# Optimization experiments

Measured on AMD Instinct MI355X. Metric: run time of the kernel, lower is better.

The kernel has to match this reference:

```python
import jax, jax.numpy as jnp
import numpy as np

B, S, D = 2, 2048, 2048
H, G = 32, 8           # num_heads, num_groups
HD = D // H            # head_dim = 64
GS = H // G            # group_size = 4


def setup_inputs() -> dict:
    key = jax.random.key(0)
    ks = jax.random.split(key, 11)
    s = 0.02
    return {
        "x": jax.random.normal(ks[0], (B, S, D), dtype=jnp.float32),
        "kv": jax.random.normal(ks[1], (B, S, D), dtype=jnp.float32),
        "Wq": jax.random.normal(ks[2], (D, D), dtype=jnp.float32) * s,
        "bq": jnp.zeros((D,), dtype=jnp.float32),
        "Wk": jax.random.normal(ks[3], (D, G * HD), dtype=jnp.float32) * s,
        "bk": jnp.zeros((G * HD,), dtype=jnp.float32),
        "Wv": jax.random.normal(ks[4], (D, G * HD), dtype=jnp.float32) * s,
        "bv": jnp.zeros((G * HD,), dtype=jnp.float32),
        "Wo": jax.random.normal(ks[5], (D, D), dtype=jnp.float32) * s,
        "bo": jnp.zeros((D,), dtype=jnp.float32),
        "expanding_context": 0,
    }


def reference(x, kv, Wq, bq, Wk, bk, Wv, bv, Wo, bo, expanding_context):
    # expanding_context is ignored when use_kv_cache=False (matches torch module)
    b, s, d = x.shape
    q = (x @ Wq + bq).reshape(b, s, H, HD).transpose(0, 2, 1, 3)      # [B,H,S,HD]
    k = (kv @ Wk + bk).reshape(b, s, G, HD).transpose(0, 2, 1, 3)     # [B,G,S,HD]
    v = (kv @ Wv + bv).reshape(b, s, G, HD).transpose(0, 2, 1, 3)     # [B,G,S,HD]
    # repeat_interleave KV heads to match query heads
    k = jnp.repeat(k, GS, axis=1)                                      # [B,H,S,HD]
    v = jnp.repeat(v, GS, axis=1)
    scale = 1.0 / jnp.sqrt(jnp.array(HD, dtype=x.dtype))
    scores = jnp.einsum("bhqd,bhkd->bhqk", q, k) * scale              # [B,H,S,S]
    causal = jnp.tril(jnp.ones((s, s), dtype=bool))                    # True where allowed
    scores = jnp.where(causal[None, None], scores, jnp.finfo(x.dtype).min)
    attn = jax.nn.softmax(scores, axis=-1)
    out = jnp.einsum("bhqk,bhkd->bhqd", attn, v)                      # [B,H,S,HD]
    out = out.transpose(0, 2, 1, 3).reshape(b, s, D)                  # [B,S,D]
    return out @ Wo + bo
```

## Files before the change

kernel.cpp:

```cpp
#include <hip/hip_runtime.h>
#include <hip/hip_bf16.h>
#include <stdint.h>

namespace {
constexpr int CB = 2, CS = 2048, CD = 2048, CH = 32, CG = 8, CHD = 64, CGS = 4;

typedef __bf16 bf16x8 __attribute__((ext_vector_type(8)));
typedef float f32x4 __attribute__((ext_vector_type(4)));
typedef float f32x16 __attribute__((ext_vector_type(16)));
typedef uint32_t u32x4 __attribute__((ext_vector_type(4)));

__device__ inline uint16_t f2bf(float f) {
  uint32_t u = __float_as_uint(f);
  u += 0x7fffu + ((u >> 16) & 1u);
  return (uint16_t)(u >> 16);
}

__device__ inline void gload_lds16(const void* g, void* l) {
  __builtin_amdgcn_global_load_lds(
      (const __attribute__((address_space(1))) void*)g,
      (__attribute__((address_space(3))) void*)l, 16, 0, 0);
}

__device__ inline uint32_t cvtpk_bf16(float lo, float hi) {
  uint32_t r;
  asm("v_cvt_pk_bf16_f32 %0, %1, %2" : "=v"(r) : "v"(lo), "v"(hi));
  return r;
}
__device__ inline void pl32swap(uint32_t& a, uint32_t& b) {
  asm("v_permlane32_swap_b32 %0, %1" : "+v"(a), "+v"(b));
}
}

__global__ __launch_bounds__(256) void cast_both_kernel(
    const float* __restrict__ x, const float* __restrict__ kv,
    uint16_t* __restrict__ xb, uint16_t* __restrict__ kvb, int nel) {
  int i = (blockIdx.x * 256 + threadIdx.x) * 4;
  const float* in;
  uint16_t* out;
  if (i < nel) { in = x + i; out = xb + i; }
  else         { in = kv + (i - nel); out = kvb + (i - nel); }
  const float4 v = *(const float4*)in;
  ushort4 o;
  o.x = f2bf(v.x); o.y = f2bf(v.y); o.z = f2bf(v.z); o.w = f2bf(v.w);
  *(ushort4*)out = o;
}

__global__ __launch_bounds__(256) void transpose_all_kernel(
    const float* __restrict__ Wq, const float* __restrict__ Wk,
    const float* __restrict__ Wv, const float* __restrict__ Wo,
    uint16_t* __restrict__ out) {
  __shared__ uint16_t tile[32][33];
  const int gn0 = blockIdx.x * 32;
  const int k0 = blockIdx.y * 32;
  const float* in;
  int Nr, start;
  if (gn0 < 2048)      { in = Wq; Nr = 2048; start = 0; }
  else if (gn0 < 2560) { in = Wk; Nr = 512;  start = 2048; }
  else if (gn0 < 3072) { in = Wv; Nr = 512;  start = 2560; }
  else                 { in = Wo; Nr = 2048; start = 3072; }
  const int n0 = gn0 - start;
  const int tx = threadIdx.x & 31, tg = threadIdx.x >> 5;
#pragma unroll
  for (int rr = 0; rr < 4; ++rr) {
    int k = tg * 4 + rr;
    tile[k][tx] = f2bf(in[(size_t)(k0 + k) * Nr + n0 + tx]);
  }
  __syncthreads();
#pragma unroll
  for (int rr = 0; rr < 4; ++rr) {
    int n = tg * 4 + rr;
    out[(size_t)(gn0 + n) * CD + k0 + tx] = tile[tx][n];
  }
}

__global__ __launch_bounds__(512, 2) void gemm_qkv_kernel(
    const uint16_t* __restrict__ xb, const uint16_t* __restrict__ kvb,
    const uint16_t* __restrict__ WT,
    const float* __restrict__ bq, const float* __restrict__ bk,
    const float* __restrict__ bv,
    uint16_t* __restrict__ Qb, uint16_t* __restrict__ Kb,
    uint16_t* __restrict__ VTb) {
  constexpr int BM = 256, BN = 256, BK = 32, K = 2048, NT = K / BK;
  constexpr int ASZ = BM * BK;
  constexpr int BSZ = BN * BK;
  constexpr int BUFSZ = ASZ + BSZ;
  __shared__ uint16_t smem[3 * BUFSZ];
  const int tid = threadIdx.x;
  const int w = tid >> 6, l = tid & 63;
  const int wr = w >> 2, wc = w & 3;
  const int l15 = l & 15, lq = l >> 4;

  const int gx = gridDim.x;
  int bid = blockIdx.y * gx + blockIdx.x;
  const int nwg = gx * gridDim.y;
  bid = (bid & 7) * (nwg >> 3) + (bid >> 3);
  const int m0 = (bid / gx) * BM, n0 = (bid % gx) * BN;
  const uint16_t* A = (n0 < 2048) ? xb : kvb;

  auto stage = [&](int buf, int kt) {
    uint16_t* base = smem + buf * BUFSZ;
    const int k0 = kt * BK;
#pragma unroll
    for (int i = 0; i < 2; ++i) {
      int g = i * 512 + tid;
      int row = g >> 2, slot = g & 3;
      int kq = slot ^ (row & 3);
      gload_lds16(A + (size_t)(m0 + row) * K + k0 + kq * 8, base + g * 8);
    }
#pragma unroll
    for (int i = 0; i < 2; ++i) {
      int g = i * 512 + tid;
      int row = g >> 2, slot = g & 3;
      int kq = slot ^ (row & 3);
      gload_lds16(WT + (size_t)(n0 + row) * K + k0 + kq * 8,
                  base + ASZ + g * 8);
    }
  };

  int aOff[8], bOff[4];
#pragma unroll
  for (int m = 0; m < 8; ++m) {
    int row = wr * 128 + m * 16 + l15;
    aOff[m] = (row * BK + (lq ^ (row & 3)) * 8) * 2;
  }
#pragma unroll
  for (int n = 0; n < 4; ++n) {
    int row = wc * 64 + n * 16 + l15;
    bOff[n] = ASZ * 2 + (row * BK + (lq ^ (row & 3)) * 8) * 2;
  }

  f32x4 acc[8][4] = {};

  stage(0, 0);
  stage(1, 1);

  int bt = 0, bs = 2;
  for (int t = 0; t < NT; ++t) {
    if (t < NT - 1) asm volatile("s_waitcnt vmcnt(4)" ::: "memory");
    else            asm volatile("s_waitcnt vmcnt(0)" ::: "memory");
    __builtin_amdgcn_s_barrier();
    asm volatile("" ::: "memory");

    const char* buf = (const char*)(smem + bt * BUFSZ);
    bf16x8 af[8], bfr[4];
#pragma unroll
    for (int m = 0; m < 8; ++m) af[m] = *(const bf16x8*)(buf + aOff[m]);
#pragma unroll
    for (int n = 0; n < 4; ++n) bfr[n] = *(const bf16x8*)(buf + bOff[n]);

    if (t + 2 < NT) stage(bs, t + 2);

    __builtin_amdgcn_s_setprio(1);
#pragma unroll
    for (int m = 0; m < 8; ++m)
#pragma unroll
      for (int n = 0; n < 4; ++n)
        acc[m][n] = __builtin_amdgcn_mfma_f32_16x16x32_bf16(
            af[m], bfr[n], acc[m][n], 0, 0, 0);
    __builtin_amdgcn_s_setprio(0);

    bt = bt == 2 ? 0 : bt + 1;
    bs = bs == 2 ? 0 : bs + 1;
  }

#pragma unroll
  for (int m = 0; m < 8; ++m)
#pragma unroll
    for (int n = 0; n < 4; ++n)
#pragma unroll
      for (int r = 0; r < 4; ++r) {
        int gm = m0 + wr * 128 + m * 16 + lq * 4 + r;
        int gn = n0 + wc * 64 + n * 16 + l15;
        int b = gm >> 11, s = gm & (CS - 1);
        if (n0 < 2048) {
          float v = (acc[m][n][r] + bq[gn]) * (0.125f * 1.44269504088896340736f);
          int h = gn >> 6, hd = gn & 63;
          Qb[(((size_t)(b * CH + h)) * CS + s) * CHD + hd] = f2bf(v);
        } else if (n0 < 2560) {
          int gn2 = gn - 2048;
          float v = acc[m][n][r] + bk[gn2];
          int gh = gn2 >> 6, hd = gn2 & 63;
          Kb[(((size_t)(b * CG + gh)) * CS + s) * CHD + hd] = f2bf(v);
        } else {
          int gn2 = gn - 2560;
          float v = acc[m][n][r] + bv[gn2];
          int gh = gn2 >> 6, hd = gn2 & 63;
          VTb[(((size_t)(b * CG + gh)) * CHD + hd) * CS + s] = f2bf(v);
        }
      }
}

__global__ __launch_bounds__(512, 2) void gemm_out_kernel(
    const uint16_t* __restrict__ A, const uint16_t* __restrict__ Bt,
    const float* __restrict__ bias, float* __restrict__ Cout,
    int M, int N, int Kdim) {
  constexpr int BM = 256, BN = 128, BK = 32, K = 2048, NT = K / BK;
  constexpr int ASZ = BM * BK;
  constexpr int BSZ = BN * BK;
  constexpr int BUFSZ = ASZ + BSZ;
  __shared__ uint16_t smem[3 * BUFSZ];
  const int tid = threadIdx.x;
  const int w = tid >> 6, l = tid & 63;
  const int wr = w >> 2, wc = w & 3;
  const int l15 = l & 15, lq = l >> 4;

  const int gx = gridDim.x;
  int bid = blockIdx.y * gx + blockIdx.x;
  const int nwg = gx * gridDim.y;
  bid = (bid & 7) * (nwg >> 3) + (bid >> 3);
  const int m0 = (bid / gx) * BM, n0 = (bid % gx) * BN;

  auto stage = [&](int buf, int kt) {
    uint16_t* base = smem + buf * BUFSZ;
    const int k0 = kt * BK;
#pragma unroll
    for (int i = 0; i < 2; ++i) {
      int g = i * 512 + tid;
      int row = g >> 2, slot = g & 3;
      int kq = slot ^ (row & 3);
      gload_lds16(A + (size_t)(m0 + row) * K + k0 + kq * 8, base + g * 8);
    }
    {
      int g = tid;
      int row = g >> 2, slot = g & 3;
      int kq = slot ^ (row & 3);
      gload_lds16(Bt + (size_t)(n0 + row) * K + k0 + kq * 8,
                  base + ASZ + g * 8);
    }
  };

  int aOff[8], bOff[2];
#pragma unroll
  for (int m = 0; m < 8; ++m) {
    int row = wr * 128 + m * 16 + l15;
    aOff[m] = (row * BK + (lq ^ (row & 3)) * 8) * 2;
  }
#pragma unroll
  for (int n = 0; n < 2; ++n) {
    int row = wc * 32 + n * 16 + l15;
    bOff[n] = ASZ * 2 + (row * BK + (lq ^ (row & 3)) * 8) * 2;
  }

  f32x4 acc[8][2] = {};

  stage(0, 0);
  stage(1, 1);

  int bt = 0, bs = 2;
  for (int t = 0; t < NT; ++t) {
    if (t < NT - 1) asm volatile("s_waitcnt vmcnt(3)" ::: "memory");
    else            asm volatile("s_waitcnt vmcnt(0)" ::: "memory");
    __builtin_amdgcn_s_barrier();
    asm volatile("" ::: "memory");

    const char* buf = (const char*)(smem + bt * BUFSZ);
    bf16x8 af[8], bfr[2];
#pragma unroll
    for (int m = 0; m < 8; ++m) af[m] = *(const bf16x8*)(buf + aOff[m]);
#pragma unroll
    for (int n = 0; n < 2; ++n) bfr[n] = *(const bf16x8*)(buf + bOff[n]);

    if (t + 2 < NT) stage(bs, t + 2);

    __builtin_amdgcn_s_setprio(1);
#pragma unroll
    for (int m = 0; m < 8; ++m)
#pragma unroll
      for (int n = 0; n < 2; ++n)
        acc[m][n] = __builtin_amdgcn_mfma_f32_16x16x32_bf16(
            af[m], bfr[n], acc[m][n], 0, 0, 0);
    __builtin_amdgcn_s_setprio(0);

    bt = bt == 2 ? 0 : bt + 1;
    bs = bs == 2 ? 0 : bs + 1;
  }

#pragma unroll
  for (int m = 0; m < 8; ++m)
#pragma unroll
    for (int n = 0; n < 2; ++n)
#pragma unroll
      for (int r = 0; r < 4; ++r) {
        int gm = m0 + wr * 128 + m * 16 + lq * 4 + r;
        int gn = n0 + wc * 32 + n * 16 + l15;
        Cout[(size_t)gm * N + gn] = acc[m][n][r] + bias[gn];
      }
}

__global__ __launch_bounds__(256) void flash_attn_kernel(
    const uint16_t* __restrict__ Q, const uint16_t* __restrict__ K,
    const uint16_t* __restrict__ VT, uint16_t* __restrict__ Aout) {
  constexpr int NQB = CS / 128;
  __shared__ __align__(16) uint16_t Ksm[2][64 * 64];
  __shared__ __align__(16) uint16_t Vsm[2][64 * 64];
  const int tid = threadIdx.x, w = tid >> 6, l = tid & 63;
  const int l31 = l & 31, hi = l >> 5;
  const int x = blockIdx.x;
  const int h = blockIdx.y, b = blockIdx.z, g = h >> 2;

  const uint16_t* Qbase = Q + ((size_t)(b * CH + h)) * CS * CHD;
  const uint16_t* Kbase = K + ((size_t)(b * CG + g)) * CS * CHD;
  const uint16_t* Vbase = VT + ((size_t)(b * CG + g)) * CHD * CS;

  const int srow = tid >> 3, sslot = tid & 7;
  const int skq = sslot ^ (srow & 7);
  const uint16_t* kSrc0 = Kbase + (size_t)srow * CHD + skq * 8;
  const uint16_t* kSrc1 = kSrc0 + 32 * CHD;
  const uint16_t* vSrc0 = Vbase + (size_t)srow * CS + skq * 8;
  const uint16_t* vSrc1 = vSrc0 + 32 * CS;
  uint16_t* kDst0 = &Ksm[0][0] + tid * 8;
  uint16_t* vDst0 = &Vsm[0][0] + tid * 8;

  int qkOff[2][4];
#pragma unroll
  for (int c = 0; c < 2; ++c)
#pragma unroll
    for (int kc = 0; kc < 4; ++kc) {
      int row = c * 32 + l31;
      qkOff[c][kc] = ((row * 64 + kc * 16 + hi * 8) * 2) ^ ((row & 7) << 4);
    }

  auto stage = [&](int buf, int kt) {
    const size_t ko = (size_t)kt * 64 * CHD;
    const int vo = kt * 64;
    uint16_t* kd = kDst0 + buf * 64 * 64;
    uint16_t* vd = vDst0 + buf * 64 * 64;
    gload_lds16(kSrc0 + ko, kd);
    gload_lds16(kSrc1 + ko, kd + 2048);
    gload_lds16(vSrc0 + vo, vd);
    gload_lds16(vSrc1 + vo, vd + 2048);
  };

#pragma unroll 1
  for (int job = 0; job < 2; ++job) {
    const int qb = job == 0 ? (NQB - 1 - x) : x;
    const int qrow = qb * 128 + w * 32 + l31;
    const int wtop = qb * 128 + w * 32 + 31;

    bf16x8 qf[4];
#pragma unroll
    for (int kc = 0; kc < 4; ++kc)
      qf[kc] = *(const bf16x8*)(Qbase + (size_t)qrow * CHD + kc * 16 + hi * 8);

    f32x16 o0 = {}, o1 = {};
    float mrun = -3e38f, lrun = 0.f;
    const int nt = 2 * qb + 2;

    stage(0, 0);
    asm volatile("s_waitcnt vmcnt(0)" ::: "memory");
    __syncthreads();

    for (int kt = 0; kt < nt; ++kt) {
      const int cur = kt & 1;
      if (kt + 1 < nt) stage(cur ^ 1, kt + 1);

      if (kt * 64 <= wtop) {
        const char* ksmb = (const char*)Ksm[cur];
        const char* vsmb = (const char*)Vsm[cur];

        f32x16 p0 = {}, p1 = {};
        __builtin_amdgcn_s_setprio(1);
#pragma unroll
        for (int kc = 0; kc < 4; ++kc) {
          bf16x8 ka0 = *(const bf16x8*)(ksmb + qkOff[0][kc]);
          bf16x8 ka1 = *(const bf16x8*)(ksmb + qkOff[1][kc]);
          p0 = __builtin_amdgcn_mfma_f32_32x32x16_bf16(ka0, qf[kc], p0, 0, 0, 0);
          p1 = __builtin_amdgcn_mfma_f32_32x32x16_bf16(ka1, qf[kc], p1, 0, 0, 0);
        }
        __builtin_amdgcn_s_setprio(0);

        const bool need_mask = (kt * 64 + 63 > qb * 128 + w * 32);
        float pmax = -3e38f;
        if (need_mask) {
#pragma unroll
          for (int r = 0; r < 16; ++r) {
            int keyb = kt * 64 + (r & 3) + 8 * (r >> 2) + 4 * hi;
            if (keyb > qrow) p0[r] = -3e38f;
            if (keyb + 32 > qrow) p1[r] = -3e38f;
          }
        }
#pragma unroll
        for (int r = 0; r < 16; ++r) {
          pmax = fmaxf(pmax, p0[r]);
          pmax = fmaxf(pmax, p1[r]);
        }
        pmax = fmaxf(pmax, __shfl_xor(pmax, 32));

        if (!__all(pmax <= mrun + 8.f)) {
          float mnew = fmaxf(mrun, pmax);
          float alpha = __builtin_amdgcn_exp2f(mrun - mnew);
#pragma unroll
          for (int r = 0; r < 16; ++r) { o0[r] *= alpha; o1[r] *= alpha; }
          lrun *= alpha;
          mrun = mnew;
        }
        float s = 0.f;
#pragma unroll
        for (int r = 0; r < 16; ++r) {
          float e0 = __builtin_amdgcn_exp2f(p0[r] - mrun);
          float e1 = __builtin_amdgcn_exp2f(p1[r] - mrun);
          p0[r] = e0; p1[r] = e1;
          s += e0 + e1;
        }
        s += __shfl_xor(s, 32);
        lrun += s;

        u32x4 paw[4];
#pragma unroll
        for (int k = 0; k < 4; ++k) {
          const int base = (k & 1) * 8;
          const f32x16& pc = (k >> 1) ? p1 : p0;
          uint32_t c01 = cvtpk_bf16(pc[base + 0], pc[base + 1]);
          uint32_t c23 = cvtpk_bf16(pc[base + 2], pc[base + 3]);
          uint32_t c45 = cvtpk_bf16(pc[base + 4], pc[base + 5]);
          uint32_t c67 = cvtpk_bf16(pc[base + 6], pc[base + 7]);
          pl32swap(c01, c45);
          pl32swap(c23, c67);
          paw[k] = (u32x4){c01, c23, c45, c67};
        }

        __builtin_amdgcn_s_setprio(1);
#pragma unroll
        for (int ks = 0; ks < 4; ++ks) {
          bf16x8 vb0 = *(const bf16x8*)(vsmb + qkOff[0][ks]);
          bf16x8 vb1 = *(const bf16x8*)(vsmb + qkOff[1][ks]);
          bf16x8 pb = __builtin_bit_cast(bf16x8, paw[ks]);
          o0 = __builtin_amdgcn_mfma_f32_32x32x16_bf16(vb0, pb, o0, 0, 0, 0);
          o1 = __builtin_amdgcn_mfma_f32_32x32x16_bf16(vb1, pb, o1, 0, 0, 0);
        }
        __builtin_amdgcn_s_setprio(0);
      }

      asm volatile("s_waitcnt vmcnt(0)" ::: "memory");
      __syncthreads();
    }

    float invl = 1.f / lrun;
    uint16_t* orow = Aout + ((size_t)b * CS + qrow) * CD + (size_t)h * CHD;
#pragma unroll
    for (int k = 0; k < 8; ++k) {
      int reg = 2 * k;
      int hd = (reg & 3) + 8 * (reg >> 2) + 4 * hi;
      *(uint32_t*)(orow + hd) = cvtpk_bf16(o0[reg] * invl, o0[reg + 1] * invl);
      *(uint32_t*)(orow + hd + 32) = cvtpk_bf16(o1[reg] * invl, o1[reg + 1] * invl);
    }
  }
}

extern "C" void kernel_launch(void* const* d_in, const int* in_sizes, int n_in,
                              void* d_out, int out_size, void* d_ws, size_t ws_size,
                              hipStream_t stream) {
  const float* x = (const float*)d_in[0];
  const float* kv = (const float*)d_in[1];
  const float* Wq = (const float*)d_in[2];
  const float* bq = (const float*)d_in[3];
  const float* Wk = (const float*)d_in[4];
  const float* bk = (const float*)d_in[5];
  const float* Wv = (const float*)d_in[6];
  const float* bv = (const float*)d_in[7];
  const float* Wo = (const float*)d_in[8];
  const float* bo = (const float*)d_in[9];
  float* out = (float*)d_out;

  char* ws = (char*)d_ws;
  uint16_t* xb = (uint16_t*)ws;   ws += (size_t)CB * CS * CD * 2;
  uint16_t* kvb = (uint16_t*)ws;  ws += (size_t)CB * CS * CD * 2;
  uint16_t* WqT = (uint16_t*)ws;  ws += (size_t)CD * CD * 2;
  uint16_t* WkT = (uint16_t*)ws;  ws += (size_t)(CG * CHD) * CD * 2;
  uint16_t* WvT = (uint16_t*)ws;  ws += (size_t)(CG * CHD) * CD * 2;
  uint16_t* WoT = (uint16_t*)ws;  ws += (size_t)CD * CD * 2;
  uint16_t* Qb = (uint16_t*)ws;   ws += (size_t)CB * CH * CS * CHD * 2;
  uint16_t* Kb = (uint16_t*)ws;   ws += (size_t)CB * CG * CS * CHD * 2;
  uint16_t* VTb = (uint16_t*)ws;  ws += (size_t)CB * CG * CHD * CS * 2;
  uint16_t* attnb = (uint16_t*)ws;
  (void)WkT; (void)WvT;

  const int NTOK = CB * CS;
  const int nel = CB * CS * CD;

  cast_both_kernel<<<2 * nel / 4 / 256, 256, 0, stream>>>(x, kv, xb, kvb, nel);
  transpose_all_kernel<<<dim3(5120 / 32, CD / 32), 256, 0, stream>>>(
      Wq, Wk, Wv, Wo, WqT);

  gemm_qkv_kernel<<<dim3(3072 / 256, NTOK / 256), 512, 0, stream>>>(
      xb, kvb, WqT, bq, bk, bv, Qb, Kb, VTb);

  flash_attn_kernel<<<dim3(CS / 256, CH, CB), 256, 0, stream>>>(Qb, Kb, VTb, attnb);

  gemm_out_kernel<<<dim3(CD / 128, NTOK / 256), 512, 0, stream>>>(
      attnb, WoT, bo, out, NTOK, CD, CD);
}
```

Before: 217.6 us.

## Split GEMM k-step into two half-phases with interleaved staging and new LDS swizzle

Both projection GEMM kernels now split each k-iteration into two halves. A-tile prefetch is issued after the first half's fragment loads and B-tile prefetch after the second half's, with an extra barrier in between. This spreads global-to-LDS traffic across the MFMA work and lowers register pressure from fragments. The LDS XOR swizzle also changes from row&3 to (row>>1)&3 to cut bank conflicts on the 16-byte reads. The extra barrier per iteration adds sync cost. The wait counts at loop top are unchanged even though issue order now differs, so prefetch accounting may be tighter.

```diff
diff --git a/kernel.cpp b/kernel.cpp
--- a/kernel.cpp
+++ b/kernel.cpp
@@ -98,21 +98,25 @@
   const int m0 = (bid / gx) * BM, n0 = (bid % gx) * BN;
   const uint16_t* A = (n0 < 2048) ? xb : kvb;
 
-  auto stage = [&](int buf, int kt) {
+  auto stageA = [&](int buf, int kt) {
     uint16_t* base = smem + buf * BUFSZ;
     const int k0 = kt * BK;
 #pragma unroll
     for (int i = 0; i < 2; ++i) {
       int g = i * 512 + tid;
       int row = g >> 2, slot = g & 3;
-      int kq = slot ^ (row & 3);
+      int kq = slot ^ ((row >> 1) & 3);
       gload_lds16(A + (size_t)(m0 + row) * K + k0 + kq * 8, base + g * 8);
     }
+  };
+  auto stageB = [&](int buf, int kt) {
+    uint16_t* base = smem + buf * BUFSZ;
+    const int k0 = kt * BK;
 #pragma unroll
     for (int i = 0; i < 2; ++i) {
       int g = i * 512 + tid;
       int row = g >> 2, slot = g & 3;
-      int kq = slot ^ (row & 3);
+      int kq = slot ^ ((row >> 1) & 3);
       gload_lds16(WT + (size_t)(n0 + row) * K + k0 + kq * 8,
                   base + ASZ + g * 8);
     }
@@ -122,18 +126,18 @@
 #pragma unroll
   for (int m = 0; m < 8; ++m) {
     int row = wr * 128 + m * 16 + l15;
-    aOff[m] = (row * BK + (lq ^ (row & 3)) * 8) * 2;
+    aOff[m] = (row * BK + (lq ^ ((row >> 1) & 3)) * 8) * 2;
   }
 #pragma unroll
   for (int n = 0; n < 4; ++n) {
     int row = wc * 64 + n * 16 + l15;
-    bOff[n] = ASZ * 2 + (row * BK + (lq ^ (row & 3)) * 8) * 2;
+    bOff[n] = ASZ * 2 + (row * BK + (lq ^ ((row >> 1) & 3)) * 8) * 2;
   }
 
   f32x4 acc[8][4] = {};
 
-  stage(0, 0);
-  stage(1, 1);
+  stageA(0, 0); stageB(0, 0);
+  stageA(1, 1); stageB(1, 1);
 
   int bt = 0, bs = 2;
   for (int t = 0; t < NT; ++t) {
@@ -143,21 +147,35 @@
     asm volatile("" ::: "memory");
 
     const char* buf = (const char*)(smem + bt * BUFSZ);
-    bf16x8 af[8], bfr[4];
-#pragma unroll
-    for (int m = 0; m < 8; ++m) af[m] = *(const bf16x8*)(buf + aOff[m]);
+
+    bf16x8 af[4], bfr[4];
+#pragma unroll
+    for (int m = 0; m < 4; ++m) af[m] = *(const bf16x8*)(buf + aOff[m]);
 #pragma unroll
     for (int n = 0; n < 4; ++n) bfr[n] = *(const bf16x8*)(buf + bOff[n]);
-
-    if (t + 2 < NT) stage(bs, t + 2);
-
+    if (t + 2 < NT) stageA(bs, t + 2);
     __builtin_amdgcn_s_setprio(1);
 #pragma unroll
-    for (int m = 0; m < 8; ++m)
+    for (int m = 0; m < 4; ++m)
 #pragma unroll
       for (int n = 0; n < 4; ++n)
         acc[m][n] = __builtin_amdgcn_mfma_f32_16x16x32_bf16(
             af[m], bfr[n], acc[m][n], 0, 0, 0);
+    __builtin_amdgcn_s_setprio(0);
+    __builtin_amdgcn_s_barrier();
+    asm volatile("" ::: "memory");
+
+    bf16x8 af2[4];
+#pragma unroll
+    for (int m = 0; m < 4; ++m) af2[m] = *(const bf16x8*)(buf + aOff[4 + m]);
+    if (t + 2 < NT) stageB(bs, t + 2);
+    __builtin_amdgcn_s_setprio(1);
+#pragma unroll
+    for (int m = 0; m < 4; ++m)
+#pragma unroll
+      for (int n = 0; n < 4; ++n)
+        acc[4 + m][n] = __builtin_amdgcn_mfma_f32_16x16x32_bf16(
+            af2[m], bfr[n], acc[4 + m][n], 0, 0, 0);
     __builtin_amdgcn_s_setprio(0);
 
     bt = bt == 2 ? 0 : bt + 1;
@@ -211,41 +229,43 @@
   bid = (bid & 7) * (nwg >> 3) + (bid >> 3);
   const int m0 = (bid / gx) * BM, n0 = (bid % gx) * BN;
 
-  auto stage = [&](int buf, int kt) {
+  auto stageA = [&](int buf, int kt) {
     uint16_t* base = smem + buf * BUFSZ;
     const int k0 = kt * BK;
 #pragma unroll
     for (int i = 0; i < 2; ++i) {
       int g = i * 512 + tid;
       int row = g >> 2, slot = g & 3;
-      int kq = slot ^ (row & 3);
+      int kq = slot ^ ((row >> 1) & 3);
       gload_lds16(A + (size_t)(m0 + row) * K + k0 + kq * 8, base + g * 8);
     }
-    {
-      int g = tid;
-      int row = g >> 2, slot = g & 3;
-      int kq = slot ^ (row & 3);
-      gload_lds16(Bt + (size_t)(n0 + row) * K + k0 + kq * 8,
-                  base + ASZ + g * 8);
-    }
+  };
+  auto stageB = [&](int buf, int kt) {
+    uint16_t* base = smem + buf * BUFSZ;
+    const int k0 = kt * BK;
+    int g = tid;
+    int row = g >> 2, slot = g & 3;
+    int kq = slot ^ ((row >> 1) & 3);
+    gload_lds16(Bt + (size_t)(n0 + row) * K + k0 + kq * 8,
+                base + ASZ + g * 8);
   };
 
   int aOff[8], bOff[2];
 #pragma unroll
   for (int m = 0; m < 8; ++m) {
     int row = wr * 128 + m * 16 + l15;
-    aOff[m] = (row * BK + (lq ^ (row & 3)) * 8) * 2;
+    aOff[m] = (row * BK + (lq ^ ((row >> 1) & 3)) * 8) * 2;
   }
 #pragma unroll
   for (int n = 0; n < 2; ++n) {
     int row = wc * 32 + n * 16 + l15;
-    bOff[n] = ASZ * 2 + (row * BK + (lq ^ (row & 3)) * 8) * 2;
+    bOff[n] = ASZ * 2 + (row * BK + (lq ^ ((row >> 1) & 3)) * 8) * 2;
   }
 
   f32x4 acc[8][2] = {};
 
-  stage(0, 0);
-  stage(1, 1);
+  stageA(0, 0); stageB(0, 0);
+  stageA(1, 1); stageB(1, 1);
 
   int bt = 0, bs = 2;
   for (int t = 0; t < NT; ++t) {
@@ -255,21 +275,35 @@
     asm volatile("" ::: "memory");
 
     const char* buf = (const char*)(smem + bt * BUFSZ);
-    bf16x8 af[8], bfr[2];
-#pragma unroll
-    for (int m = 0; m < 8; ++m) af[m] = *(const bf16x8*)(buf + aOff[m]);
+
+    bf16x8 af[4], bfr[2];
+#pragma unroll
+    for (int m = 0; m < 4; ++m) af[m] = *(const bf16x8*)(buf + aOff[m]);
 #pragma unroll
     for (int n = 0; n < 2; ++n) bfr[n] = *(const bf16x8*)(buf + bOff[n]);
-
-    if (t + 2 < NT) stage(bs, t + 2);
-
+    if (t + 2 < NT) stageA(bs, t + 2);
     __builtin_amdgcn_s_setprio(1);
 #pragma unroll
-    for (int m = 0; m < 8; ++m)
+    for (int m = 0; m < 4; ++m)
 #pragma unroll
       for (int n = 0; n < 2; ++n)
         acc[m][n] = __builtin_amdgcn_mfma_f32_16x16x32_bf16(
             af[m], bfr[n], acc[m][n], 0, 0, 0);
+    __builtin_amdgcn_s_setprio(0);
+    __builtin_amdgcn_s_barrier();
+    asm volatile("" ::: "memory");
+
+    bf16x8 af2[4];
+#pragma unroll
+    for (int m = 0; m < 4; ++m) af2[m] = *(const bf16x8*)(buf + aOff[4 + m]);
+    if (t + 2 < NT) stageB(bs, t + 2);
+    __builtin_amdgcn_s_setprio(1);
+#pragma unroll
+    for (int m = 0; m < 4; ++m)
+#pragma unroll
+      for (int n = 0; n < 2; ++n)
+        acc[4 + m][n] = __builtin_amdgcn_mfma_f32_16x16x32_bf16(
+            af2[m], bfr[n], acc[4 + m][n], 0, 0, 0);
     __builtin_amdgcn_s_setprio(0);
 
     bt = bt == 2 ? 0 : bt + 1;
```

Measured after the change: 211.0 us. -3.0%, faster.
